# Kernel tuning notes

Hardware: AMD Instinct MI355X
Metric: run time of the kernel (lower is better)

## Reference

```python
import jax, jax.numpy as jnp
import numpy as np

B, N, C_IN, C_OUT = 4, 2048, 1024, 1024


def setup_inputs() -> dict:
    key = jax.random.key(0)
    ks = jax.random.split(key, 4)
    scale = 1.0 / np.sqrt(C_IN)
    return {
        "hidden_states": jax.random.normal(ks[0], (B, N, C_IN), dtype=jnp.float32),
        "Wq": jax.random.normal(ks[1], (C_OUT, C_IN), dtype=jnp.float32) * scale,
        "bq": jnp.zeros((C_OUT,), dtype=jnp.float32),
        "Wk": jax.random.normal(ks[2], (C_OUT, C_IN), dtype=jnp.float32) * scale,
        "bk": jnp.zeros((C_OUT,), dtype=jnp.float32),
        "Wv": jax.random.normal(ks[3], (C_OUT, C_IN), dtype=jnp.float32) * scale,
        "bv": jnp.zeros((C_OUT,), dtype=jnp.float32),
    }


def reference(hidden_states, Wq, bq, Wk, bk, Wv, bv):
    # torch nn.Linear: y = x @ W.T + b
    Q = jnp.einsum("bnc,dc->bnd", hidden_states, Wq) + bq
    K = jnp.einsum("bnc,dc->bnd", hidden_states, Wk) + bk
    V = jnp.einsum("bnc,dc->bnd", hidden_states, Wv) + bv
    d_k = K.shape[-1]
    scores = jnp.einsum("bnd,bmd->bnm", Q, K) * (d_k ** -0.5)  # [B,N,N]
    attention = jax.nn.softmax(scores, axis=-1)
    out = jnp.einsum("bnm,bmd->bnd", attention, V)
    return (out, attention)
```

## Files before the change

kernel.cpp:

```cpp
#include <hip/hip_runtime.h>
#include <cstdint>

typedef __attribute__((ext_vector_type(8))) short bf16x8;
typedef __attribute__((ext_vector_type(4))) float f32x4;

__device__ __forceinline__ unsigned short f2bf(float v) {
  unsigned u = __builtin_bit_cast(unsigned, v);
  u += 0x7FFFu + ((u >> 16) & 1u);
  return (unsigned short)(u >> 16);
}

__device__ __forceinline__ void gload16(const unsigned short* g, unsigned short* l) {
  __builtin_amdgcn_global_load_lds(
      (const __attribute__((address_space(1))) void*)(uintptr_t)g,
      (__attribute__((address_space(3))) void*)(uint32_t)(uintptr_t)l,
      16, 0, 0);
}

#define BAR()   asm volatile("s_barrier" ::: "memory")
#define LGKM0() asm volatile("s_waitcnt lgkmcnt(0)" ::: "memory")
#define VM4()   asm volatile("s_waitcnt vmcnt(4)" ::: "memory")
#define VM0()   asm volatile("s_waitcnt vmcnt(0)" ::: "memory")

__device__ __forceinline__ void gemm_core(
    const unsigned short* __restrict__ A, const unsigned short* __restrict__ B,
    int lda, int ldb, int NT,
    unsigned short* lds, f32x4 acc[4][4])
{
  const int tid  = threadIdx.x;
  const int w    = tid >> 6;
  const int lane = tid & 63;
  const int wr   = w >> 2;
  const int wc   = w & 3;
  const int lrow = lane & 15;
  const int kq   = lane >> 4;

  const int srow = tid >> 3;
  const int schk = ((tid & 7) ^ (srow & 7)) * 8;
  const unsigned short* gA = A + (long)srow * lda + schk;
  const unsigned short* gB = B + (long)srow * ldb + schk;
  unsigned short* const stg = lds + w * 512;

  const int aoff  = (wr * 64 + lrow) * 64;
  const int boff  = ((wc & 1) * 64 + lrow) * 64;
  const int bunit = wc >> 1;
  const int pc0 = ((0 + kq) ^ (lrow & 7)) * 8;
  const int pc1 = ((4 + kq) ^ (lrow & 7)) * 8;

  gload16(const_cast<unsigned short*>(gB) - 0,          stg);
  gload16(const_cast<unsigned short*>(gB) + (long)64 * ldb,  stg + 4096);
  gload16(const_cast<unsigned short*>(gB) + (long)128 * ldb, stg + 8192);
  gload16(const_cast<unsigned short*>(gB) + (long)192 * ldb, stg + 8192 + 4096);
  gload16(const_cast<unsigned short*>(gA),                   stg + 2 * 8192);
  gload16(const_cast<unsigned short*>(gA) + (long)64 * lda,  stg + 2 * 8192 + 4096);
  gload16(const_cast<unsigned short*>(gB) + 64,              stg + 3 * 8192);
  gload16(const_cast<unsigned short*>(gB) + 64 + (long)64 * ldb,  stg + 3 * 8192 + 4096);
  gload16(const_cast<unsigned short*>(gB) + 64 + (long)128 * ldb, stg + 4 * 8192);
  gload16(const_cast<unsigned short*>(gB) + 64 + (long)192 * ldb, stg + 4 * 8192 + 4096);
  VM4();
  BAR();

  for (int t = 0; t < NT; ++t) {
    const int r3 = 3 * (t & 1);
    const unsigned short* lA = lds + (r3 + 2) * 8192 + aoff;
    const unsigned short* lB = lds + (r3 + bunit) * 8192 + boff;

    bf16x8 bfr[4][2], af[2][2];
#pragma unroll
    for (int j = 0; j < 4; ++j) {
      bfr[j][0] = *(const bf16x8*)(lB + j * 1024 + pc0);
      bfr[j][1] = *(const bf16x8*)(lB + j * 1024 + pc1);
    }
#pragma unroll
    for (int i = 0; i < 2; ++i) {
      af[i][0] = *(const bf16x8*)(lA + i * 1024 + pc0);
      af[i][1] = *(const bf16x8*)(lA + i * 1024 + pc1);
    }
    if (t + 1 < NT) {
      const unsigned short* s = gA + (t + 1) * 64;
      unsigned short* d = stg + (3 * ((t + 1) & 1) + 2) * 8192;
      gload16(const_cast<unsigned short*>(s),                  d);
      gload16(const_cast<unsigned short*>(s) + (long)64 * lda, d + 4096);
    }
    BAR();
    LGKM0();
    __builtin_amdgcn_s_setprio(1);
#pragma unroll
    for (int i = 0; i < 2; ++i)
#pragma unroll
      for (int j = 0; j < 4; ++j) {
        acc[i][j] = __builtin_amdgcn_mfma_f32_16x16x32_bf16(af[i][0], bfr[j][0], acc[i][j], 0, 0, 0);
        acc[i][j] = __builtin_amdgcn_mfma_f32_16x16x32_bf16(af[i][1], bfr[j][1], acc[i][j], 0, 0, 0);
      }
    __builtin_amdgcn_s_setprio(0);
    BAR();

#pragma unroll
    for (int i = 0; i < 2; ++i) {
      af[i][0] = *(const bf16x8*)(lA + (i + 2) * 1024 + pc0);
      af[i][1] = *(const bf16x8*)(lA + (i + 2) * 1024 + pc1);
    }
    if (t + 2 < NT) {
      const unsigned short* s = gB + (t + 2) * 64;
      unsigned short* d = stg + r3 * 8192;
      gload16(const_cast<unsigned short*>(s),                   d);
      gload16(const_cast<unsigned short*>(s) + (long)64 * ldb,  d + 4096);
      gload16(const_cast<unsigned short*>(s) + (long)128 * ldb, d + 8192);
      gload16(const_cast<unsigned short*>(s) + (long)192 * ldb, d + 8192 + 4096);
    }
    BAR();
    LGKM0();
    __builtin_amdgcn_s_setprio(1);
#pragma unroll
    for (int i = 0; i < 2; ++i)
#pragma unroll
      for (int j = 0; j < 4; ++j) {
        acc[i + 2][j] = __builtin_amdgcn_mfma_f32_16x16x32_bf16(af[i][0], bfr[j][0], acc[i + 2][j], 0, 0, 0);
        acc[i + 2][j] = __builtin_amdgcn_mfma_f32_16x16x32_bf16(af[i][1], bfr[j][1], acc[i + 2][j], 0, 0, 0);
      }
    __builtin_amdgcn_s_setprio(0);
    if (t == NT - 2) { VM0(); } else { VM4(); }
    BAR();
  }
}

__global__ __launch_bounds__(512, 2) void gemm_qkv(
    const unsigned short* __restrict__ xh,
    const unsigned short* __restrict__ wh,
    const float* __restrict__ bq, const float* __restrict__ bk, const float* __restrict__ bv,
    unsigned short* __restrict__ Qh, unsigned short* __restrict__ Kh,
    unsigned short* __restrict__ Vth)
{
  __shared__ __align__(16) unsigned short lds[49152];
  const int Mblk = blockIdx.x * 128;
  const int sel  = blockIdx.y >> 2;
  const int nb   = blockIdx.y & 3;

  const unsigned short* A = xh + (long)Mblk * 1024;
  const unsigned short* B = wh + sel * 1048576 + (long)(nb * 256) * 1024;
  const float* bias = (sel == 0) ? bq : (sel == 1) ? bk : bv;

  f32x4 acc[4][4] = {};
  gemm_core(A, B, 1024, 1024, 16, lds, acc);

  const int lane = threadIdx.x & 63, w = threadIdx.x >> 6;
  const int wr = w >> 2, wc = w & 3;
  const int lrow = lane & 15, kq = lane >> 4;

#pragma unroll
  for (int i = 0; i < 4; ++i) {
#pragma unroll
    for (int j = 0; j < 4; ++j) {
      const int col = nb * 256 + wc * 64 + j * 16 + lrow;
      const float bsv = bias[col];
#pragma unroll
      for (int r = 0; r < 4; ++r) {
        const int tok = Mblk + wr * 64 + i * 16 + kq * 4 + r;
        const unsigned short h = f2bf(acc[i][j][r] + bsv);
        if (sel == 2) {
          Vth[(long)(tok >> 11) * 2097152 + (long)col * 2048 + (tok & 2047)] = h;
        } else if (sel == 0) {
          Qh[(long)tok * 1024 + col] = h;
        } else {
          Kh[(long)tok * 1024 + col] = h;
        }
      }
    }
  }
}

__global__ __launch_bounds__(512, 2) void gemm_f32out(
    const unsigned short* __restrict__ A, const unsigned short* __restrict__ B,
    int lda, int ldb, int NT,
    long sA, long sB, float* __restrict__ C, int ldc, long sC, float alpha)
{
  __shared__ __align__(16) unsigned short lds[49152];
  const int Mblk = blockIdx.x * 128;
  const int Nblk = blockIdx.y * 256;
  const long z = blockIdx.z;
  const unsigned short* Ab = A + z * sA + (long)Mblk * lda;
  const unsigned short* Bb = B + z * sB + (long)Nblk * ldb;
  float* Cb = C + z * sC;

  f32x4 acc[4][4] = {};
  gemm_core(Ab, Bb, lda, ldb, NT, lds, acc);

  const int lane = threadIdx.x & 63, w = threadIdx.x >> 6;
  const int wr = w >> 2, wc = w & 3;
  const int lrow = lane & 15, kq = lane >> 4;
#pragma unroll
  for (int i = 0; i < 4; ++i)
#pragma unroll
    for (int j = 0; j < 4; ++j)
#pragma unroll
      for (int r = 0; r < 4; ++r) {
        const int row = Mblk + wr * 64 + i * 16 + kq * 4 + r;
        const int col = Nblk + wc * 64 + j * 16 + lrow;
        Cb[(long)row * ldc + col] = alpha * acc[i][j][r];
      }
}

__global__ __launch_bounds__(256) void softmax_rows(
    float* __restrict__ S, unsigned short* __restrict__ Ph)
{
  __shared__ float red[4];
  const long row = blockIdx.x;
  float* rp = S + row * 2048;
  const int t = threadIdx.x;

  float x[8];
  *(float4*)&x[0] = reinterpret_cast<const float4*>(rp)[t];
  *(float4*)&x[4] = reinterpret_cast<const float4*>(rp)[t + 256];

  float m = x[0];
#pragma unroll
  for (int i = 1; i < 8; ++i) m = fmaxf(m, x[i]);
  for (int o = 32; o; o >>= 1) m = fmaxf(m, __shfl_xor(m, o, 64));
  if ((t & 63) == 0) red[t >> 6] = m;
  __syncthreads();
  m = fmaxf(fmaxf(red[0], red[1]), fmaxf(red[2], red[3]));
  __syncthreads();

  float s = 0.f;
#pragma unroll
  for (int i = 0; i < 8; ++i) { x[i] = expf(x[i] - m); s += x[i]; }
  for (int o = 32; o; o >>= 1) s += __shfl_xor(s, o, 64);
  if ((t & 63) == 0) red[t >> 6] = s;
  __syncthreads();
  s = (red[0] + red[1]) + (red[2] + red[3]);
  const float inv = 1.0f / s;

#pragma unroll
  for (int i = 0; i < 8; ++i) x[i] *= inv;
  reinterpret_cast<float4*>(rp)[t]       = *(float4*)&x[0];
  reinterpret_cast<float4*>(rp)[t + 256] = *(float4*)&x[4];

  const long b0 = row * 2048 + t * 4;
#pragma unroll
  for (int k = 0; k < 4; ++k) Ph[b0 + k] = f2bf(x[k]);
  const long b1 = row * 2048 + 1024 + t * 4;
#pragma unroll
  for (int k = 0; k < 4; ++k) Ph[b1 + k] = f2bf(x[4 + k]);
}

__global__ __launch_bounds__(256) void to_bf16(
    const float* __restrict__ x, unsigned short* __restrict__ hi, int n4)
{
  int i = blockIdx.x * 256 + threadIdx.x;
  const int stride = gridDim.x * 256;
  for (; i < n4; i += stride) {
    const float4 v = reinterpret_cast<const float4*>(x)[i];
    ushort4 h;
    h.x = f2bf(v.x); h.y = f2bf(v.y); h.z = f2bf(v.z); h.w = f2bf(v.w);
    reinterpret_cast<ushort4*>(hi)[i] = h;
  }
}

extern "C" void kernel_launch(void* const* d_in, const int* in_sizes, int n_in,
                              void* d_out, int out_size, void* d_ws, size_t ws_size,
                              hipStream_t stream)
{
  const float* x  = (const float*)d_in[0];
  const float* Wq = (const float*)d_in[1];
  const float* bq = (const float*)d_in[2];
  const float* Wk = (const float*)d_in[3];
  const float* bk = (const float*)d_in[4];
  const float* Wv = (const float*)d_in[5];
  const float* bv = (const float*)d_in[6];

  float* out  = (float*)d_out;
  float* attn = (float*)d_out + 8388608;

  unsigned short* ws  = (unsigned short*)d_ws;
  unsigned short* xh  = ws;
  unsigned short* wh  = xh + 8388608;
  unsigned short* Qh  = wh + 3145728;
  unsigned short* Kh  = Qh + 8388608;
  unsigned short* Vth = Kh + 8388608;
  unsigned short* Ph  = Vth + 8388608;

  to_bf16<<<2048, 256, 0, stream>>>(x, xh, 2097152);
  to_bf16<<<512, 256, 0, stream>>>(Wq, wh, 262144);
  to_bf16<<<512, 256, 0, stream>>>(Wk, wh + 1048576, 262144);
  to_bf16<<<512, 256, 0, stream>>>(Wv, wh + 2097152, 262144);

  gemm_qkv<<<dim3(64, 12), 512, 0, stream>>>(xh, wh, bq, bk, bv, Qh, Kh, Vth);

  gemm_f32out<<<dim3(16, 8, 4), 512, 0, stream>>>(Qh, Kh, 1024, 1024, 16,
      2097152L, 2097152L, attn, 2048, 4194304L, 0.03125f);

  softmax_rows<<<8192, 256, 0, stream>>>(attn, Ph);

  gemm_f32out<<<dim3(16, 4, 4), 512, 0, stream>>>(Ph, Vth, 2048, 2048, 32,
      4194304L, 2097152L, out, 1024, 2097152L, 1.0f);
}
```

Measured before the change: 321.6 us.

## Enlarge GEMM tiles to 256x256 with four-phase pipelined K loop

The shared GEMM core now computes 256x256 output tiles instead of 128x256. Each wave holds 8x4 accumulator fragments, and the K loop is split into four phases that interleave LDS reads, staged global-to-LDS loads and MFMA blocks. LDS grows to 128KB per block and the launch grids are halved along M. The aim is more operand reuse per byte loaded from global memory. In exchange, register pressure and LDS use rise sharply, which likely means one block per CU despite launch_bounds(512,2), and the smaller grids (for example 256 blocks for the PV GEMM) may underfill the 256 CUs.

```diff
diff --git a/kernel.cpp b/kernel.cpp
--- a/kernel.cpp
+++ b/kernel.cpp
@@ -19,13 +19,12 @@
 
 #define BAR()   asm volatile("s_barrier" ::: "memory")
 #define LGKM0() asm volatile("s_waitcnt lgkmcnt(0)" ::: "memory")
-#define VM4()   asm volatile("s_waitcnt vmcnt(4)" ::: "memory")
-#define VM0()   asm volatile("s_waitcnt vmcnt(0)" ::: "memory")
+#define VMW(N)  asm volatile("s_waitcnt vmcnt(" #N ")" ::: "memory")
 
 __device__ __forceinline__ void gemm_core(
     const unsigned short* __restrict__ A, const unsigned short* __restrict__ B,
     int lda, int ldb, int NT,
-    unsigned short* lds, f32x4 acc[4][4])
+    unsigned short* lds, f32x4 acc[8][4])
 {
   const int tid  = threadIdx.x;
   const int w    = tid >> 6;
@@ -41,87 +40,68 @@
   const unsigned short* gB = B + (long)srow * ldb + schk;
   unsigned short* const stg = lds + w * 512;
 
-  const int aoff  = (wr * 64 + lrow) * 64;
-  const int boff  = ((wc & 1) * 64 + lrow) * 64;
-  const int bunit = wc >> 1;
   const int pc0 = ((0 + kq) ^ (lrow & 7)) * 8;
   const int pc1 = ((4 + kq) ^ (lrow & 7)) * 8;
 
-  gload16(const_cast<unsigned short*>(gB) - 0,          stg);
-  gload16(const_cast<unsigned short*>(gB) + (long)64 * ldb,  stg + 4096);
-  gload16(const_cast<unsigned short*>(gB) + (long)128 * ldb, stg + 8192);
-  gload16(const_cast<unsigned short*>(gB) + (long)192 * ldb, stg + 8192 + 4096);
-  gload16(const_cast<unsigned short*>(gA),                   stg + 2 * 8192);
-  gload16(const_cast<unsigned short*>(gA) + (long)64 * lda,  stg + 2 * 8192 + 4096);
-  gload16(const_cast<unsigned short*>(gB) + 64,              stg + 3 * 8192);
-  gload16(const_cast<unsigned short*>(gB) + 64 + (long)64 * ldb,  stg + 3 * 8192 + 4096);
-  gload16(const_cast<unsigned short*>(gB) + 64 + (long)128 * ldb, stg + 4 * 8192);
-  gload16(const_cast<unsigned short*>(gB) + 64 + (long)192 * ldb, stg + 4 * 8192 + 4096);
-  VM4();
+  #define STG(g, ld, H, t, s) do { \
+    gload16((g) + (long)(H)      * (ld) + (t) * 64, stg + (s) * 8192); \
+    gload16((g) + (long)((H)+64) * (ld) + (t) * 64, stg + (s) * 8192 + 4096); \
+  } while (0)
+
+  STG(gB, ldb, 0,   0, 0);
+  STG(gB, ldb, 128, 0, 1);
+  STG(gA, lda, 0,   0, 2);
+  STG(gA, lda, 128, 0, 3);
+  STG(gB, ldb, 0,   1, 4);
+  STG(gB, ldb, 128, 1, 5);
+  VMW(4);
   BAR();
 
   for (int t = 0; t < NT; ++t) {
-    const int r3 = 3 * (t & 1);
-    const unsigned short* lA = lds + (r3 + 2) * 8192 + aoff;
-    const unsigned short* lB = lds + (r3 + bunit) * 8192 + boff;
+    const int base = (t & 1) * 32768;
+    const unsigned short* lA = lds + base + (2 + wr) * 8192 + lrow * 64;
+    const unsigned short* lB = lds + base + (wc >> 1) * 8192 + ((wc & 1) * 64 + lrow) * 64;
+    const bool doA = (t + 1 < NT);
+    const bool doB = (t + 2 < NT);
 
     bf16x8 bfr[4][2], af[2][2];
 #pragma unroll
-    for (int j = 0; j < 4; ++j) {
-      bfr[j][0] = *(const bf16x8*)(lB + j * 1024 + pc0);
-      bfr[j][1] = *(const bf16x8*)(lB + j * 1024 + pc1);
+    for (int p = 0; p < 4; ++p) {
+      if (p == 0) {
+#pragma unroll
+        for (int j = 0; j < 4; ++j) {
+          bfr[j][0] = *(const bf16x8*)(lB + j * 1024 + pc0);
+          bfr[j][1] = *(const bf16x8*)(lB + j * 1024 + pc1);
+        }
+      }
+#pragma unroll
+      for (int i = 0; i < 2; ++i) {
+        af[i][0] = *(const bf16x8*)(lA + (2 * p + i) * 1024 + pc0);
+        af[i][1] = *(const bf16x8*)(lA + (2 * p + i) * 1024 + pc1);
+      }
+      if (p == 0 && doA) STG(gA, lda, 0,   t + 1, ((t + 1) & 1) * 4 + 2);
+      if (p == 1 && doA) STG(gA, lda, 128, t + 1, ((t + 1) & 1) * 4 + 3);
+      if (p == 2 && doB) STG(gB, ldb, 0,   t + 2, (t & 1) * 4 + 0);
+      if (p == 3 && doB) STG(gB, ldb, 128, t + 2, (t & 1) * 4 + 1);
+      BAR();
+      LGKM0();
+      __builtin_amdgcn_s_setprio(1);
+#pragma unroll
+      for (int i = 0; i < 2; ++i)
+#pragma unroll
+        for (int j = 0; j < 4; ++j) {
+          acc[2 * p + i][j] = __builtin_amdgcn_mfma_f32_16x16x32_bf16(af[i][0], bfr[j][0], acc[2 * p + i][j], 0, 0, 0);
+          acc[2 * p + i][j] = __builtin_amdgcn_mfma_f32_16x16x32_bf16(af[i][1], bfr[j][1], acc[2 * p + i][j], 0, 0, 0);
+        }
+      __builtin_amdgcn_s_setprio(0);
+      if (p == 3) {
+        if (t < NT - 2)       { VMW(4); }
+        else if (t == NT - 2) { VMW(0); }
+      }
+      BAR();
     }
-#pragma unroll
-    for (int i = 0; i < 2; ++i) {
-      af[i][0] = *(const bf16x8*)(lA + i * 1024 + pc0);
-      af[i][1] = *(const bf16x8*)(lA + i * 1024 + pc1);
-    }
-    if (t + 1 < NT) {
-      const unsigned short* s = gA + (t + 1) * 64;
-      unsigned short* d = stg + (3 * ((t + 1) & 1) + 2) * 8192;
-      gload16(const_cast<unsigned short*>(s),                  d);
-      gload16(const_cast<unsigned short*>(s) + (long)64 * lda, d + 4096);
-    }
-    BAR();
-    LGKM0();
-    __builtin_amdgcn_s_setprio(1);
-#pragma unroll
-    for (int i = 0; i < 2; ++i)
-#pragma unroll
-      for (int j = 0; j < 4; ++j) {
-        acc[i][j] = __builtin_amdgcn_mfma_f32_16x16x32_bf16(af[i][0], bfr[j][0], acc[i][j], 0, 0, 0);
-        acc[i][j] = __builtin_amdgcn_mfma_f32_16x16x32_bf16(af[i][1], bfr[j][1], acc[i][j], 0, 0, 0);
-      }
-    __builtin_amdgcn_s_setprio(0);
-    BAR();
-
-#pragma unroll
-    for (int i = 0; i < 2; ++i) {
-      af[i][0] = *(const bf16x8*)(lA + (i + 2) * 1024 + pc0);
-      af[i][1] = *(const bf16x8*)(lA + (i + 2) * 1024 + pc1);
-    }
-    if (t + 2 < NT) {
-      const unsigned short* s = gB + (t + 2) * 64;
-      unsigned short* d = stg + r3 * 8192;
-      gload16(const_cast<unsigned short*>(s),                   d);
-      gload16(const_cast<unsigned short*>(s) + (long)64 * ldb,  d + 4096);
-      gload16(const_cast<unsigned short*>(s) + (long)128 * ldb, d + 8192);
-      gload16(const_cast<unsigned short*>(s) + (long)192 * ldb, d + 8192 + 4096);
-    }
-    BAR();
-    LGKM0();
-    __builtin_amdgcn_s_setprio(1);
-#pragma unroll
-    for (int i = 0; i < 2; ++i)
-#pragma unroll
-      for (int j = 0; j < 4; ++j) {
-        acc[i + 2][j] = __builtin_amdgcn_mfma_f32_16x16x32_bf16(af[i][0], bfr[j][0], acc[i + 2][j], 0, 0, 0);
-        acc[i + 2][j] = __builtin_amdgcn_mfma_f32_16x16x32_bf16(af[i][1], bfr[j][1], acc[i + 2][j], 0, 0, 0);
-      }
-    __builtin_amdgcn_s_setprio(0);
-    if (t == NT - 2) { VM0(); } else { VM4(); }
-    BAR();
   }
+  #undef STG
 }
 
 __global__ __launch_bounds__(512, 2) void gemm_qkv(
@@ -131,8 +111,8 @@
     unsigned short* __restrict__ Qh, unsigned short* __restrict__ Kh,
     unsigned short* __restrict__ Vth)
 {
-  __shared__ __align__(16) unsigned short lds[49152];
-  const int Mblk = blockIdx.x * 128;
+  __shared__ __align__(16) unsigned short lds[65536];
+  const int Mblk = blockIdx.x * 256;
   const int sel  = blockIdx.y >> 2;
   const int nb   = blockIdx.y & 3;
 
@@ -140,7 +120,7 @@
   const unsigned short* B = wh + sel * 1048576 + (long)(nb * 256) * 1024;
   const float* bias = (sel == 0) ? bq : (sel == 1) ? bk : bv;
 
-  f32x4 acc[4][4] = {};
+  f32x4 acc[8][4] = {};
   gemm_core(A, B, 1024, 1024, 16, lds, acc);
 
   const int lane = threadIdx.x & 63, w = threadIdx.x >> 6;
@@ -148,14 +128,14 @@
   const int lrow = lane & 15, kq = lane >> 4;
 
 #pragma unroll
-  for (int i = 0; i < 4; ++i) {
+  for (int i = 0; i < 8; ++i) {
 #pragma unroll
     for (int j = 0; j < 4; ++j) {
       const int col = nb * 256 + wc * 64 + j * 16 + lrow;
       const float bsv = bias[col];
 #pragma unroll
       for (int r = 0; r < 4; ++r) {
-        const int tok = Mblk + wr * 64 + i * 16 + kq * 4 + r;
+        const int tok = Mblk + wr * 128 + i * 16 + kq * 4 + r;
         const unsigned short h = f2bf(acc[i][j][r] + bsv);
         if (sel == 2) {
           Vth[(long)(tok >> 11) * 2097152 + (long)col * 2048 + (tok & 2047)] = h;
@@ -174,27 +154,27 @@
     int lda, int ldb, int NT,
     long sA, long sB, float* __restrict__ C, int ldc, long sC, float alpha)
 {
-  __shared__ __align__(16) unsigned short lds[49152];
-  const int Mblk = blockIdx.x * 128;
+  __shared__ __align__(16) unsigned short lds[65536];
+  const int Mblk = blockIdx.x * 256;
   const int Nblk = blockIdx.y * 256;
   const long z = blockIdx.z;
   const unsigned short* Ab = A + z * sA + (long)Mblk * lda;
   const unsigned short* Bb = B + z * sB + (long)Nblk * ldb;
   float* Cb = C + z * sC;
 
-  f32x4 acc[4][4] = {};
+  f32x4 acc[8][4] = {};
   gemm_core(Ab, Bb, lda, ldb, NT, lds, acc);
 
   const int lane = threadIdx.x & 63, w = threadIdx.x >> 6;
   const int wr = w >> 2, wc = w & 3;
   const int lrow = lane & 15, kq = lane >> 4;
 #pragma unroll
-  for (int i = 0; i < 4; ++i)
+  for (int i = 0; i < 8; ++i)
 #pragma unroll
     for (int j = 0; j < 4; ++j)
 #pragma unroll
       for (int r = 0; r < 4; ++r) {
-        const int row = Mblk + wr * 64 + i * 16 + kq * 4 + r;
+        const int row = Mblk + wr * 128 + i * 16 + kq * 4 + r;
         const int col = Nblk + wc * 64 + j * 16 + lrow;
         Cb[(long)row * ldc + col] = alpha * acc[i][j][r];
       }
@@ -284,13 +264,13 @@
   to_bf16<<<512, 256, 0, stream>>>(Wk, wh + 1048576, 262144);
   to_bf16<<<512, 256, 0, stream>>>(Wv, wh + 2097152, 262144);
 
-  gemm_qkv<<<dim3(64, 12), 512, 0, stream>>>(xh, wh, bq, bk, bv, Qh, Kh, Vth);
-
-  gemm_f32out<<<dim3(16, 8, 4), 512, 0, stream>>>(Qh, Kh, 1024, 1024, 16,
+  gemm_qkv<<<dim3(32, 12), 512, 0, stream>>>(xh, wh, bq, bk, bv, Qh, Kh, Vth);
+
+  gemm_f32out<<<dim3(8, 8, 4), 512, 0, stream>>>(Qh, Kh, 1024, 1024, 16,
       2097152L, 2097152L, attn, 2048, 4194304L, 0.03125f);
 
   softmax_rows<<<8192, 256, 0, stream>>>(attn, Ph);
 
-  gemm_f32out<<<dim3(16, 4, 4), 512, 0, stream>>>(Ph, Vth, 2048, 2048, 32,
+  gemm_f32out<<<dim3(8, 4, 4), 512, 0, stream>>>(Ph, Vth, 2048, 2048, 32,
       4194304L, 2097152L, out, 1024, 2097152L, 1.0f);
 }
```

Measured after the change: 349.9 us. +8.8%, slower.
